# Optimization experiments

Measured on AMD Instinct MI355X. Metric: run time of the kernel, lower is better.

Reference implementation:

```python
import jax, jax.numpy as jnp
import numpy as np

EPS = 1e-5  # torch LayerNorm default

def setup_inputs() -> dict:
    key = jax.random.key(0)
    k1, k2, k3 = jax.random.split(key, 3)
    x = jax.random.normal(k1, (8, 256, 256, 256), dtype=jnp.float32)
    w_size = 256
    bound = 1.0 / np.sqrt(w_size)
    W = jax.random.uniform(k2, (w_size, w_size), dtype=jnp.float32, minval=-bound, maxval=bound)
    b = jax.random.uniform(k3, (w_size,), dtype=jnp.float32, minval=-bound, maxval=bound)
    return {"x": x, "W": W, "b": b}

def reference(x, W, b):
    # x: [B, 2C, G, Wd]; chunk along channel dim
    u, v = jnp.split(x, 2, axis=1)
    # LayerNorm over all non-batch dims (weight=1, bias=0 since module is
    # constructed fresh inside forward)
    mean = jnp.mean(v, axis=(1, 2, 3), keepdims=True)
    var = jnp.mean(jnp.square(v - mean), axis=(1, 2, 3), keepdims=True)
    v = (v - mean) * jax.lax.rsqrt(var + EPS)
    # Linear along last dim: y = v @ W.T + b
    v = jnp.einsum('bcgw,ow->bcgo', v, W) + b
    return u * (v + 1.0)
```

## Files before the change

### kernel.cpp

```cpp
#include <hip/hip_runtime.h>
#include <hip/hip_bf16.h>

typedef __attribute__((ext_vector_type(8))) short short8_t;
typedef __attribute__((ext_vector_type(4))) float f32x4;

__device__ __forceinline__ short f2bf(float f) {
    union { float f; unsigned u; } v; v.f = f;
    unsigned r = (v.u + 0x7FFFu + ((v.u >> 16) & 1u)) >> 16;
    return (short)r;
}

#define N_PER_BATCH 8388608.0f
#define LDR 264

__global__ __launch_bounds__(256) void stats_partial(const float* __restrict__ x,
                                                     float2* __restrict__ partials) {
    int bid = blockIdx.x;
    int batch = bid >> 8;
    int blk   = bid & 255;
    const float* base = x + ((size_t)batch << 24) + (1u << 23) + ((size_t)blk << 15);
    int tid = threadIdx.x;
    float s1 = 0.f, s2 = 0.f;
    #pragma unroll
    for (int i = 0; i < 32; ++i) {
        float4 v = *reinterpret_cast<const float4*>(base + (size_t)(i * 256 + tid) * 4);
        s1 += v.x + v.y + v.z + v.w;
        s2 += v.x * v.x + v.y * v.y + v.z * v.z + v.w * v.w;
    }
    #pragma unroll
    for (int off = 32; off; off >>= 1) {
        s1 += __shfl_down(s1, off);
        s2 += __shfl_down(s2, off);
    }
    __shared__ float2 red[4];
    if ((tid & 63) == 0) red[tid >> 6] = make_float2(s1, s2);
    __syncthreads();
    if (tid == 0) {
        float a1 = 0.f, a2 = 0.f;
        #pragma unroll
        for (int w = 0; w < 4; ++w) { a1 += red[w].x; a2 += red[w].y; }
        partials[bid] = make_float2(a1, a2);
    }
}

__global__ __launch_bounds__(256) void stats_final(const float2* __restrict__ partials,
                                                   float2* __restrict__ stats) {
    int batch = blockIdx.x;
    int tid = threadIdx.x;
    float2 p = partials[(batch << 8) + tid];
    float s1 = p.x, s2 = p.y;
    #pragma unroll
    for (int off = 32; off; off >>= 1) {
        s1 += __shfl_down(s1, off);
        s2 += __shfl_down(s2, off);
    }
    __shared__ float2 red[4];
    if ((tid & 63) == 0) red[tid >> 6] = make_float2(s1, s2);
    __syncthreads();
    if (tid == 0) {
        float a1 = 0.f, a2 = 0.f;
        #pragma unroll
        for (int w = 0; w < 4; ++w) { a1 += red[w].x; a2 += red[w].y; }
        float mean = a1 / N_PER_BATCH;
        float var  = a2 / N_PER_BATCH - mean * mean;
        stats[batch] = make_float2(mean, rsqrtf(var + 1e-5f));
    }
}

__global__ __launch_bounds__(1024, 4) void fused_gemm(const float* __restrict__ x,
                                                      const float* __restrict__ W,
                                                      const float* __restrict__ bias,
                                                      const float2* __restrict__ stats,
                                                      float* __restrict__ out) {
    __shared__ short vt[2][16 * LDR];
    const int tid  = threadIdx.x;
    const int wid  = tid >> 6;
    const int lane = tid & 63;
    const int l15  = lane & 15;
    const int l4   = lane >> 4;
    const int q    = l15 & 3;
    const int qg   = l15 >> 2;

    const int bi = blockIdx.x >> 5;
    const float2 ms = stats[bi];
    const float mean = ms.x, rstd = ms.y;

    short8_t bfrag[8];
    {
        const float* wbase = W + (size_t)(wid * 16 + l15) * 256 + (l4 << 3);
        #pragma unroll
        for (int kb = 0; kb < 8; ++kb) {
            float4 p0 = *reinterpret_cast<const float4*>(wbase + kb * 32);
            float4 p1 = *reinterpret_cast<const float4*>(wbase + kb * 32 + 4);
            short8_t s;
            s[0] = f2bf(p0.x); s[1] = f2bf(p0.y); s[2] = f2bf(p0.z); s[3] = f2bf(p0.w);
            s[4] = f2bf(p1.x); s[5] = f2bf(p1.y); s[6] = f2bf(p1.z); s[7] = f2bf(p1.w);
            bfrag[kb] = s;
        }
    }
    float4 bq = *reinterpret_cast<const float4*>(bias + wid * 16 + (qg << 2));
    bq.x += 1.f; bq.y += 1.f; bq.z += 1.f; bq.w += 1.f;

    const size_t row0 = (size_t)blockIdx.x << 10;
    const float* vbase = x + ((size_t)bi << 24) + (1u << 23) + ((row0 & 32767) << 8);
    const float* ubase = x + ((size_t)bi << 24) + ((row0 & 32767) << 8);
    float*       obase = out + (row0 << 8);

    const int   srow = tid >> 6;
    const int   scol = (tid & 63) << 2;
    const size_t goff = (size_t)srow * 256 + scol;
    const int   lds_w = srow * LDR + scol;

    const size_t eoff = (size_t)(l4 * 4 + q) * 256 + wid * 16 + (qg << 2);

    const int aoff = l15 * LDR + (l4 << 3);

    {
        float4 v0 = *reinterpret_cast<const float4*>(vbase + goff);
        short4 s;
        s.x = f2bf((v0.x - mean) * rstd); s.y = f2bf((v0.y - mean) * rstd);
        s.z = f2bf((v0.z - mean) * rstd); s.w = f2bf((v0.w - mean) * rstd);
        *reinterpret_cast<short4*>(&vt[0][lds_w]) = s;
    }
    __syncthreads();

    for (int t = 0; t < 64; ++t) {
        const int cur = t & 1;
        const int tn = (t < 63) ? t + 1 : 63;
        float4 vn = *reinterpret_cast<const float4*>(vbase + ((size_t)tn << 12) + goff);
        const size_t uo = ((size_t)t << 12) + eoff;
        float4 u4 = *reinterpret_cast<const float4*>(ubase + uo);

        f32x4 acc = {0.f, 0.f, 0.f, 0.f};
        #pragma unroll
        for (int kb = 0; kb < 8; ++kb) {
            short8_t a = *reinterpret_cast<const short8_t*>(&vt[cur][aoff + kb * 32]);
            acc = __builtin_amdgcn_mfma_f32_16x16x32_bf16(a, bfrag[kb], acc, 0, 0, 0);
        }

        float v0 = acc[0], v1 = acc[1], v2 = acc[2], v3 = acc[3];
        float s0 = __shfl_xor(v1, 1), s1 = __shfl_xor(v0, 1);
        float s2 = __shfl_xor(v3, 1), s3 = __shfl_xor(v2, 1);
        const bool qb0 = (q & 1);
        float w0 = qb0 ? s0 : v0;
        float w1 = qb0 ? v1 : s1;
        float w2 = qb0 ? s2 : v2;
        float w3 = qb0 ? v3 : s3;
        float t0 = __shfl_xor(w2, 2), t1 = __shfl_xor(w3, 2);
        float t2 = __shfl_xor(w0, 2), t3 = __shfl_xor(w1, 2);
        const bool qb1 = (q & 2);
        float x0 = qb1 ? t0 : w0;
        float x1 = qb1 ? t1 : w1;
        float x2 = qb1 ? w2 : t2;
        float x3 = qb1 ? w3 : t3;

        float4 o;
        o.x = u4.x * (x0 + bq.x);
        o.y = u4.y * (x1 + bq.y);
        o.z = u4.z * (x2 + bq.z);
        o.w = u4.w * (x3 + bq.w);
        *reinterpret_cast<float4*>(obase + uo) = o;

        short4 sn;
        sn.x = f2bf((vn.x - mean) * rstd); sn.y = f2bf((vn.y - mean) * rstd);
        sn.z = f2bf((vn.z - mean) * rstd); sn.w = f2bf((vn.w - mean) * rstd);
        *reinterpret_cast<short4*>(&vt[cur ^ 1][lds_w]) = sn;
        __syncthreads();
    }
}

extern "C" void kernel_launch(void* const* d_in, const int* in_sizes, int n_in,
                              void* d_out, int out_size, void* d_ws, size_t ws_size,
                              hipStream_t stream) {
    const float* x    = (const float*)d_in[0];
    const float* W    = (const float*)d_in[1];
    const float* bias = (const float*)d_in[2];
    float* out = (float*)d_out;

    float2* partials = (float2*)d_ws;
    float2* stats    = (float2*)((char*)d_ws + 16384);

    stats_partial<<<2048, 256, 0, stream>>>(x, partials);
    stats_final<<<8, 256, 0, stream>>>(partials, stats);
    fused_gemm<<<256, 1024, 0, stream>>>(x, W, bias, stats, out);
}
```

Before: 215.7 us.

## Process batches in pairs so stats pass and GEMM reuse v in cache

The launch sequence is split into four groups of two batches, each running stats, finalize and GEMM, so the v half of x read by the stats pass may still sit in the last-level cache when the GEMM reads it. The GEMM block shrinks to 512 threads, each wave computes two 16-column output tiles sharing one A fragment, and each block handles 128 rows in 8 iterations instead of 1024 rows in 64. The cost is twelve kernel launches instead of three, shorter per-block pipelines, and more registers per thread.

```diff
diff --git a/kernel.cpp b/kernel.cpp
--- a/kernel.cpp
+++ b/kernel.cpp
@@ -14,9 +14,10 @@
 #define LDR 264
 
 __global__ __launch_bounds__(256) void stats_partial(const float* __restrict__ x,
-                                                     float2* __restrict__ partials) {
+                                                     float2* __restrict__ partials,
+                                                     int batch0) {
     int bid = blockIdx.x;
-    int batch = bid >> 8;
+    int batch = batch0 + (bid >> 8);
     int blk   = bid & 255;
     const float* base = x + ((size_t)batch << 24) + (1u << 23) + ((size_t)blk << 15);
     int tid = threadIdx.x;
@@ -39,15 +40,16 @@
         float a1 = 0.f, a2 = 0.f;
         #pragma unroll
         for (int w = 0; w < 4; ++w) { a1 += red[w].x; a2 += red[w].y; }
-        partials[bid] = make_float2(a1, a2);
+        partials[((size_t)batch << 8) + blk] = make_float2(a1, a2);
     }
 }
 
 __global__ __launch_bounds__(256) void stats_final(const float2* __restrict__ partials,
-                                                   float2* __restrict__ stats) {
-    int batch = blockIdx.x;
+                                                   float2* __restrict__ stats,
+                                                   int batch0) {
+    int batch = batch0 + blockIdx.x;
     int tid = threadIdx.x;
-    float2 p = partials[(batch << 8) + tid];
+    float2 p = partials[((size_t)batch << 8) + tid];
     float s1 = p.x, s2 = p.y;
     #pragma unroll
     for (int off = 32; off; off >>= 1) {
@@ -67,11 +69,12 @@
     }
 }
 
-__global__ __launch_bounds__(1024, 4) void fused_gemm(const float* __restrict__ x,
-                                                      const float* __restrict__ W,
-                                                      const float* __restrict__ bias,
-                                                      const float2* __restrict__ stats,
-                                                      float* __restrict__ out) {
+__global__ __launch_bounds__(512, 4) void fused_gemm(const float* __restrict__ x,
+                                                     const float* __restrict__ W,
+                                                     const float* __restrict__ bias,
+                                                     const float2* __restrict__ stats,
+                                                     float* __restrict__ out,
+                                                     int batch0) {
     __shared__ short vt[2][16 * LDR];
     const int tid  = threadIdx.x;
     const int wid  = tid >> 6;
@@ -81,13 +84,14 @@
     const int q    = l15 & 3;
     const int qg   = l15 >> 2;
 
-    const int bi = blockIdx.x >> 5;
+    const int bi = batch0 + (blockIdx.x >> 8);
     const float2 ms = stats[bi];
     const float mean = ms.x, rstd = ms.y;
 
-    short8_t bfrag[8];
-    {
-        const float* wbase = W + (size_t)(wid * 16 + l15) * 256 + (l4 << 3);
+    short8_t bfrag[2][8];
+    #pragma unroll
+    for (int c = 0; c < 2; ++c) {
+        const float* wbase = W + (size_t)(wid * 32 + c * 16 + l15) * 256 + (l4 << 3);
         #pragma unroll
         for (int kb = 0; kb < 8; ++kb) {
             float4 p0 = *reinterpret_cast<const float4*>(wbase + kb * 32);
@@ -95,76 +99,105 @@
             short8_t s;
             s[0] = f2bf(p0.x); s[1] = f2bf(p0.y); s[2] = f2bf(p0.z); s[3] = f2bf(p0.w);
             s[4] = f2bf(p1.x); s[5] = f2bf(p1.y); s[6] = f2bf(p1.z); s[7] = f2bf(p1.w);
-            bfrag[kb] = s;
-        }
-    }
-    float4 bq = *reinterpret_cast<const float4*>(bias + wid * 16 + (qg << 2));
-    bq.x += 1.f; bq.y += 1.f; bq.z += 1.f; bq.w += 1.f;
-
-    const size_t row0 = (size_t)blockIdx.x << 10;
-    const float* vbase = x + ((size_t)bi << 24) + (1u << 23) + ((row0 & 32767) << 8);
-    const float* ubase = x + ((size_t)bi << 24) + ((row0 & 32767) << 8);
-    float*       obase = out + (row0 << 8);
-
-    const int   srow = tid >> 6;
-    const int   scol = (tid & 63) << 2;
-    const size_t goff = (size_t)srow * 256 + scol;
-    const int   lds_w = srow * LDR + scol;
-
-    const size_t eoff = (size_t)(l4 * 4 + q) * 256 + wid * 16 + (qg << 2);
+            bfrag[c][kb] = s;
+        }
+    }
+    float4 bq[2];
+    #pragma unroll
+    for (int c = 0; c < 2; ++c) {
+        bq[c] = *reinterpret_cast<const float4*>(bias + wid * 32 + c * 16 + (qg << 2));
+        bq[c].x += 1.f; bq[c].y += 1.f; bq[c].z += 1.f; bq[c].w += 1.f;
+    }
+
+    const size_t rowb = (size_t)(blockIdx.x & 255) * 128;
+    const float* vbase = x + ((size_t)bi << 24) + (1u << 23) + (rowb << 8);
+    const float* ubase = x + ((size_t)bi << 24) + (rowb << 8);
+    float*       obase = out + (((size_t)bi * 32768 + rowb) << 8);
+
+    int srow[2], ldsw[2]; size_t goff[2];
+    #pragma unroll
+    for (int i = 0; i < 2; ++i) {
+        int idx4 = tid + (i << 9);
+        srow[i] = idx4 >> 6;
+        int col = (idx4 & 63) << 2;
+        goff[i] = (size_t)srow[i] * 256 + col;
+        ldsw[i] = srow[i] * LDR + col;
+    }
+
+    size_t eoff[2];
+    #pragma unroll
+    for (int c = 0; c < 2; ++c)
+        eoff[c] = (size_t)(l4 * 4 + q) * 256 + wid * 32 + c * 16 + (qg << 2);
 
     const int aoff = l15 * LDR + (l4 << 3);
 
-    {
-        float4 v0 = *reinterpret_cast<const float4*>(vbase + goff);
+    #pragma unroll
+    for (int i = 0; i < 2; ++i) {
+        float4 v0 = *reinterpret_cast<const float4*>(vbase + goff[i]);
         short4 s;
         s.x = f2bf((v0.x - mean) * rstd); s.y = f2bf((v0.y - mean) * rstd);
         s.z = f2bf((v0.z - mean) * rstd); s.w = f2bf((v0.w - mean) * rstd);
-        *reinterpret_cast<short4*>(&vt[0][lds_w]) = s;
+        *reinterpret_cast<short4*>(&vt[0][ldsw[i]]) = s;
     }
     __syncthreads();
 
-    for (int t = 0; t < 64; ++t) {
+    for (int t = 0; t < 8; ++t) {
         const int cur = t & 1;
-        const int tn = (t < 63) ? t + 1 : 63;
-        float4 vn = *reinterpret_cast<const float4*>(vbase + ((size_t)tn << 12) + goff);
-        const size_t uo = ((size_t)t << 12) + eoff;
-        float4 u4 = *reinterpret_cast<const float4*>(ubase + uo);
-
-        f32x4 acc = {0.f, 0.f, 0.f, 0.f};
+        const int tn = (t < 7) ? t + 1 : 7;
+        float4 vn[2];
+        #pragma unroll
+        for (int i = 0; i < 2; ++i)
+            vn[i] = *reinterpret_cast<const float4*>(vbase + ((size_t)tn << 12) + goff[i]);
+        float4 u4[2];
+        size_t uo[2];
+        #pragma unroll
+        for (int c = 0; c < 2; ++c) {
+            uo[c] = ((size_t)t << 12) + eoff[c];
+            u4[c] = *reinterpret_cast<const float4*>(ubase + uo[c]);
+        }
+
+        f32x4 acc0 = {0.f, 0.f, 0.f, 0.f};
+        f32x4 acc1 = {0.f, 0.f, 0.f, 0.f};
         #pragma unroll
         for (int kb = 0; kb < 8; ++kb) {
             short8_t a = *reinterpret_cast<const short8_t*>(&vt[cur][aoff + kb * 32]);
-            acc = __builtin_amdgcn_mfma_f32_16x16x32_bf16(a, bfrag[kb], acc, 0, 0, 0);
-        }
-
-        float v0 = acc[0], v1 = acc[1], v2 = acc[2], v3 = acc[3];
-        float s0 = __shfl_xor(v1, 1), s1 = __shfl_xor(v0, 1);
-        float s2 = __shfl_xor(v3, 1), s3 = __shfl_xor(v2, 1);
-        const bool qb0 = (q & 1);
-        float w0 = qb0 ? s0 : v0;
-        float w1 = qb0 ? v1 : s1;
-        float w2 = qb0 ? s2 : v2;
-        float w3 = qb0 ? v3 : s3;
-        float t0 = __shfl_xor(w2, 2), t1 = __shfl_xor(w3, 2);
-        float t2 = __shfl_xor(w0, 2), t3 = __shfl_xor(w1, 2);
-        const bool qb1 = (q & 2);
-        float x0 = qb1 ? t0 : w0;
-        float x1 = qb1 ? t1 : w1;
-        float x2 = qb1 ? w2 : t2;
-        float x3 = qb1 ? w3 : t3;
-
-        float4 o;
-        o.x = u4.x * (x0 + bq.x);
-        o.y = u4.y * (x1 + bq.y);
-        o.z = u4.z * (x2 + bq.z);
-        o.w = u4.w * (x3 + bq.w);
-        *reinterpret_cast<float4*>(obase + uo) = o;
-
-        short4 sn;
-        sn.x = f2bf((vn.x - mean) * rstd); sn.y = f2bf((vn.y - mean) * rstd);
-        sn.z = f2bf((vn.z - mean) * rstd); sn.w = f2bf((vn.w - mean) * rstd);
-        *reinterpret_cast<short4*>(&vt[cur ^ 1][lds_w]) = sn;
+            acc0 = __builtin_amdgcn_mfma_f32_16x16x32_bf16(a, bfrag[0][kb], acc0, 0, 0, 0);
+            acc1 = __builtin_amdgcn_mfma_f32_16x16x32_bf16(a, bfrag[1][kb], acc1, 0, 0, 0);
+        }
+
+        #pragma unroll
+        for (int c = 0; c < 2; ++c) {
+            f32x4 acc = c ? acc1 : acc0;
+            float v0 = acc[0], v1 = acc[1], v2 = acc[2], v3 = acc[3];
+            float s0 = __shfl_xor(v1, 1), s1 = __shfl_xor(v0, 1);
+            float s2 = __shfl_xor(v3, 1), s3 = __shfl_xor(v2, 1);
+            const bool qb0 = (q & 1);
+            float w0 = qb0 ? s0 : v0;
+            float w1 = qb0 ? v1 : s1;
+            float w2 = qb0 ? s2 : v2;
+            float w3 = qb0 ? v3 : s3;
+            float t0 = __shfl_xor(w2, 2), t1 = __shfl_xor(w3, 2);
+            float t2 = __shfl_xor(w0, 2), t3 = __shfl_xor(w1, 2);
+            const bool qb1 = (q & 2);
+            float x0 = qb1 ? t0 : w0;
+            float x1 = qb1 ? t1 : w1;
+            float x2 = qb1 ? w2 : t2;
+            float x3 = qb1 ? w3 : t3;
+            float4 o;
+            o.x = u4[c].x * (x0 + bq[c].x);
+            o.y = u4[c].y * (x1 + bq[c].y);
+            o.z = u4[c].z * (x2 + bq[c].z);
+            o.w = u4[c].w * (x3 + bq[c].w);
+            *reinterpret_cast<float4*>(obase + uo[c]) = o;
+        }
+
+        #pragma unroll
+        for (int i = 0; i < 2; ++i) {
+            short4 sn;
+            sn.x = f2bf((vn[i].x - mean) * rstd); sn.y = f2bf((vn[i].y - mean) * rstd);
+            sn.z = f2bf((vn[i].z - mean) * rstd); sn.w = f2bf((vn[i].w - mean) * rstd);
+            *reinterpret_cast<short4*>(&vt[cur ^ 1][ldsw[i]]) = sn;
+        }
         __syncthreads();
     }
 }
@@ -178,9 +211,12 @@
     float* out = (float*)d_out;
 
     float2* partials = (float2*)d_ws;
-    float2* stats    = (float2*)((char*)d_ws + 16384);
-
-    stats_partial<<<2048, 256, 0, stream>>>(x, partials);
-    stats_final<<<8, 256, 0, stream>>>(partials, stats);
-    fused_gemm<<<256, 1024, 0, stream>>>(x, W, bias, stats, out);
-}
+    float2* stats    = (float2*)((char*)d_ws + 32768);
+
+    for (int g = 0; g < 4; ++g) {
+        int b0 = g * 2;
+        stats_partial<<<512, 256, 0, stream>>>(x, partials, b0);
+        stats_final<<<2, 256, 0, stream>>>(partials, stats, b0);
+        fused_gemm<<<512, 512, 0, stream>>>(x, W, bias, stats, out, b0);
+    }
+}
```

New measurement: 315.7 us. 46.4% more time.
